# Performance work log

Hardware: AMD Instinct MI355X
Metric: run time of the kernel (lower is better)

The kernel has to match this reference:

```python
import jax, jax.numpy as jnp
import numpy as np
from jax.ops import segment_sum

N = 50000        # nodes
E = 800000       # edges (avg degree 16)
H = 128          # hidden_dim
N_ITER = 2       # BCRefinement n_iterations
TIE_P = 0.05     # fraction of tie (boundary) edges


def setup_inputs() -> dict:
    key = jax.random.key(0)
    ks = jax.random.split(key, 24)
    s = 0.02
    inp = {
        'h': jax.random.normal(ks[0], (N, H), jnp.float32),
        'e': jax.random.normal(ks[1], (E, H), jnp.float32),
        'edge_attr_raw': jax.random.normal(ks[2], (E, 10), jnp.float32),
        # edge_refine: Linear(3H,2H) -> ReLU -> Linear(2H,H)
        'W_er1': s * jax.random.normal(ks[3], (3 * H, 2 * H), jnp.float32),
        'b_er1': jnp.zeros((2 * H,), jnp.float32),
        'W_er2': s * jax.random.normal(ks[4], (2 * H, H), jnp.float32),
        'b_er2': jnp.zeros((H,), jnp.float32),
        # GRUCell(H,H) torch layout: [3H, H] chunks (r, z, n)
        'W_ih': s * jax.random.normal(ks[5], (3 * H, H), jnp.float32),
        'W_hh': s * jax.random.normal(ks[6], (3 * H, H), jnp.float32),
        'b_ih': jnp.zeros((3 * H,), jnp.float32),
        'b_hh': jnp.zeros((3 * H,), jnp.float32),
        # node_neigh_fc: Linear(H,H)
        'W_nn': s * jax.random.normal(ks[7], (H, H), jnp.float32),
        'b_nn': jnp.zeros((H,), jnp.float32),
        # gate_mlp: Linear(3H,H) -> ReLU -> Linear(H,1), last bias init -2.0
        'W_g1': s * jax.random.normal(ks[8], (3 * H, H), jnp.float32),
        'b_g1': jnp.zeros((H,), jnp.float32),
        'W_g2': s * jax.random.normal(ks[9], (H, 1), jnp.float32),
        'b_g2': jnp.full((1,), -2.0, jnp.float32),
        'edge_index': jax.random.randint(ks[10], (2, E), 0, N, jnp.int32),
        'is_tie': jax.random.uniform(ks[11], (E,)) < TIE_P,
    }
    return inp


def reference(h, e, edge_attr_raw,
              W_er1, b_er1, W_er2, b_er2,
              W_ih, W_hh, b_ih, b_hh,
              W_nn, b_nn,
              W_g1, b_g1, W_g2, b_g2,
              edge_index, is_tie):
    row = edge_index[0]
    col = edge_index[1]
    tie_f = is_tie.astype(h.dtype)                        # [E]
    internal = ~is_tie

    # coupling buses: endpoints of any tie edge (tie-incidence count > 0)
    cpl_cnt = segment_sum(tie_f, row, num_segments=N) + \
              segment_sum(tie_f, col, num_segments=N)     # [N]
    is_cpl = cpl_cnt > 0

    # internal edges pointing into coupling buses; b_smooth weights w = 1/sqrt(X^2+eps)
    to_cpl = internal & is_cpl[col]
    X = jnp.abs(edge_attr_raw[:, 1])
    w = jnp.where(to_cpl, 1.0 / jnp.sqrt(X * X + 1e-6), 0.0)
    w_den = segment_sum(w, col, num_segments=N)           # [N]
    w_norm = w / (w_den[col] + 1e-6)                      # [E], zero off-mask

    deg = jnp.maximum(cpl_cnt, 1.0)                       # clamp_min(1.0)

    h_work, e_work = h, e
    for _ in range(N_ITER):
        # --- tie-edge refinement (applied only on tie edges) ---
        edge_in = jnp.concatenate([e_work, h_work[row], h_work[col]], axis=-1)  # [E,3H]
        e_ref = jax.nn.relu(edge_in @ W_er1 + b_er1) @ W_er2 + b_er2            # [E,H]
        e_work = e_work + tie_f[:, None] * e_ref

        # --- node messages from internal neighbors into coupling buses ---
        m_node_msg = h_work[row] @ W_nn + b_nn                                   # [E,H]
        m_node_all = segment_sum(m_node_msg * w_norm[:, None], col,
                                 num_segments=N)                                 # [N,H]

        # --- mean of incident tie-edge features at each node ---
        tie_e = tie_f[:, None] * e_work                                          # [E,H]
        m_edge_all = (segment_sum(tie_e, row, num_segments=N) +
                      segment_sum(tie_e, col, num_segments=N)) / deg[:, None]    # [N,H]

        # --- gating + GRU update on coupling buses ---
        gate_in = jnp.concatenate([m_edge_all, m_node_all, h_work], axis=-1)     # [N,3H]
        gate = jax.nn.sigmoid(jax.nn.relu(gate_in @ W_g1 + b_g1) @ W_g2 + b_g2)  # [N,1]
        m = m_edge_all + gate * m_node_all                                       # [N,H]

        gi = m @ W_ih.T + b_ih                                                   # [N,3H]
        gh = h_work @ W_hh.T + b_hh
        r = jax.nn.sigmoid(gi[:, :H] + gh[:, :H])
        z = jax.nn.sigmoid(gi[:, H:2 * H] + gh[:, H:2 * H])
        n = jnp.tanh(gi[:, 2 * H:] + r * gh[:, 2 * H:])
        h_new = (1.0 - z) * n + z * h_work

        h_work = jnp.where(is_cpl[:, None], h_new, h_work)
    return h_work, e_work
```

## Files before the change

kernel.cpp:

```cpp
#include <hip/hip_runtime.h>
#include <cstdint>

#define N_NODES 50000
#define N_EDGES 800000
#define HDIM    128
#define TIE_CAP 44000
#define NITER   2
#define SCAN_B  256
#define EB_CONST 3125
#define TB_CONST 172

typedef __attribute__((ext_vector_type(8))) short bf16x8;
typedef __attribute__((ext_vector_type(4))) float f32x4;

__device__ __forceinline__ uint32_t f2bf(float f) {
    uint32_t u = __builtin_bit_cast(uint32_t, f);
    return (u + 0x7fffu + ((u >> 16) & 1u)) >> 16;
}
__device__ __forceinline__ float bf2f(uint32_t b) {
    return __builtin_bit_cast(float, b << 16);
}
__device__ __forceinline__ uint32_t comb2(uint32_t me, uint32_t mn, float g) {
    float a0 = bf2f(me & 0xffffu) + g * bf2f(mn & 0xffffu);
    float a1 = bf2f(me >> 16)     + g * bf2f(mn >> 16);
    return f2bf(a0) | (f2bf(a1) << 16);
}


__device__ __forceinline__ void stage_a128(const float* __restrict__ base,
                                           const int* __restrict__ gidx,
                                           int m0, int Mlim, char* tile, int tid)
{
    const int c = tid & 15;
    #pragma unroll
    for (int p = 0; p < 4; ++p) {
        int row = p * 32 + (tid >> 4);
        int ar = m0 + row; if (ar >= Mlim) ar = Mlim - 1;
        long g = gidx ? gidx[ar] : ar;
        const float* s = base + g * HDIM + c * 4;
        float4 v0 = *(const float4*)s;
        float4 v1 = *(const float4*)(s + 64);
        uint2 w0 = make_uint2(f2bf(v0.x) | (f2bf(v0.y) << 16),
                              f2bf(v0.z) | (f2bf(v0.w) << 16));
        uint2 w1 = make_uint2(f2bf(v1.x) | (f2bf(v1.y) << 16),
                              f2bf(v1.z) | (f2bf(v1.w) << 16));
        int sw = (row & 7) << 4;
        *(uint2*)(tile + row * 256 + ((c * 8) ^ sw)) = w0;
        *(uint2*)(tile + row * 256 + ((c * 8 + 128) ^ sw)) = w1;
    }
}

__device__ __forceinline__ void stage_bf128(const uint16_t* __restrict__ base,
                                            const int* __restrict__ gidx,
                                            int m0, int Mlim, char* tile, int tid)
{
    const int c = tid & 15;
    #pragma unroll
    for (int p = 0; p < 4; ++p) {
        int row = p * 32 + (tid >> 4);
        int ar = m0 + row; if (ar >= Mlim) ar = Mlim - 1;
        long g = gidx ? gidx[ar] : ar;
        uint4 v = *(const uint4*)(base + g * HDIM + c * 8);
        *(uint4*)(tile + row * 256 + ((c * 16) ^ ((row & 7) << 4))) = v;
    }
}

__device__ __forceinline__ void stage_b128(const short* __restrict__ BT, int ldk,
                                           int n0, int k0, char* tile, int tid)
{
    const int c = tid & 15;
    #pragma unroll
    for (int p = 0; p < 4; ++p) {
        int n = p * 32 + (tid >> 4);
        uint4 v = *(const uint4*)&BT[(size_t)(n0 + n) * ldk + k0 + c * 8];
        *(uint4*)(tile + n * 256 + ((c * 16) ^ ((n & 7) << 4))) = v;
    }
}

__device__ __forceinline__ void mfma128(const char* At, const char* Bt,
                                        int wr, int wc, int lane, f32x4 acc[4][2])
{
    #pragma unroll
    for (int ks = 0; ks < 4; ++ks) {
        int kb = ks * 64 + (lane >> 4) * 16;
        bf16x8 aF[4], bF[2];
        #pragma unroll
        for (int mi = 0; mi < 4; ++mi) {
            int row = wr * 64 + mi * 16 + (lane & 15);
            aF[mi] = *(const bf16x8*)(At + row * 256 + (kb ^ ((row & 7) << 4)));
        }
        #pragma unroll
        for (int ni = 0; ni < 2; ++ni) {
            int n = wc * 32 + ni * 16 + (lane & 15);
            bF[ni] = *(const bf16x8*)(Bt + n * 256 + (kb ^ ((n & 7) << 4)));
        }
        #pragma unroll
        for (int mi = 0; mi < 4; ++mi)
            #pragma unroll
            for (int ni = 0; ni < 2; ++ni)
                acc[mi][ni] = __builtin_amdgcn_mfma_f32_16x16x32_bf16(
                    aF[mi], bF[ni], acc[mi][ni], 0, 0, 0);
    }
}

__global__ __launch_bounds__(512)
void k_tie_fused(float* __restrict__ out_e, const uint16_t* __restrict__ h_bf,
                 const int* __restrict__ tie_cnt_p,
                 const int* __restrict__ tie_list, const int* __restrict__ tie_row,
                 const int* __restrict__ tie_col,
                 const short* __restrict__ BTer1, const short* __restrict__ BTer2,
                 const float* __restrict__ b_er1, const float* __restrict__ b_er2)
{
    int cnt = *tie_cnt_p; if (cnt > TIE_CAP) cnt = TIE_CAP;
    const int m0 = blockIdx.x * 128;
    if (m0 >= cnt) return;

    __shared__ __align__(16) char At[32 * 1024];
    __shared__ __align__(16) char B0[32 * 1024];
    __shared__ __align__(16) char B1[32 * 1024];

    const int tid = threadIdx.x, lane = tid & 63;
    const int wid = tid >> 6, wr = wid >> 2, wc = wid & 3;

    f32x4 acc0[4][2] = {}, acc1[4][2] = {};
    #pragma unroll 1
    for (int c = 0; c < 3; ++c) {
        if (c == 0) stage_a128(out_e, tie_list, m0, cnt, At, tid);
        else        stage_bf128(h_bf, (c == 1) ? tie_row : tie_col, m0, cnt, At, tid);
        stage_b128(BTer1, 384, 0,   c * 128, B0, tid);
        stage_b128(BTer1, 384, 128, c * 128, B1, tid);
        __syncthreads();
        mfma128(At, B0, wr, wc, lane, acc0);
        mfma128(At, B1, wr, wc, lane, acc1);
        __syncthreads();
    }

    #pragma unroll
    for (int half = 0; half < 2; ++half) {
        char* Ct = half ? B0 : At;
        #pragma unroll
        for (int ni = 0; ni < 2; ++ni) {
            int col = wc * 32 + ni * 16 + (lane & 15);
            float bv = b_er1[half * 128 + col];
            #pragma unroll
            for (int mi = 0; mi < 4; ++mi)
                #pragma unroll
                for (int j = 0; j < 4; ++j) {
                    int rl = wr * 64 + mi * 16 + ((lane >> 4) << 2) + j;
                    float v = fmaxf((half ? acc1 : acc0)[mi][ni][j] + bv, 0.f);
                    *(uint16_t*)(Ct + rl * 256 + ((col * 2) ^ ((rl & 7) << 4))) =
                        (uint16_t)f2bf(v);
                }
        }
    }
    stage_b128(BTer2, 256, 0, 0, B1, tid);
    __syncthreads();
    f32x4 acc2[4][2] = {};
    mfma128(At, B1, wr, wc, lane, acc2);
    __syncthreads();
    stage_b128(BTer2, 256, 0, 128, B1, tid);
    __syncthreads();
    mfma128(B0, B1, wr, wc, lane, acc2);

    int col0 = wc * 32 + (lane & 15);
    float bv0 = b_er2[col0], bv1 = b_er2[col0 + 16];
    #pragma unroll
    for (int mi = 0; mi < 4; ++mi) {
        #pragma unroll
        for (int j = 0; j < 4; ++j) {
            int i = m0 + wr * 64 + mi * 16 + ((lane >> 4) << 2) + j;
            if (i < cnt) {
                int e = tie_list[i];
                #pragma unroll
                for (int ni = 0; ni < 2; ++ni) {
                    int col = col0 + ni * 16;
                    size_t eb = (size_t)e * HDIM + col;
                    out_e[eb] += acc2[mi][ni][j] + (ni ? bv1 : bv0);
                }
            }
        }
    }
}

__global__ __launch_bounds__(256)
void k_gather(const int* __restrict__ row_ptr, const int* __restrict__ csr_row,
              const float* __restrict__ csr_w, const uint16_t* __restrict__ h_bf,
              uint16_t* __restrict__ agg,
              const int* __restrict__ row_ptr2, const int* __restrict__ tcsr,
              const float* __restrict__ out_e, const float* __restrict__ deg_inv,
              uint16_t* __restrict__ m_edge_bf)
{
    int n = blockIdx.x * 4 + (threadIdx.x >> 6);
    if (n >= N_NODES) return;
    int lane = threadIdx.x & 63;

    int s = row_ptr[n], t = row_ptr[n + 1];
    float a0 = 0.f, a1 = 0.f;
    for (int j = s; j < t; ++j) {
        int r = csr_row[j];
        float w = csr_w[j];
        uint32_t v = *(const uint32_t*)(h_bf + (size_t)r * HDIM + lane * 2);
        a0 += w * bf2f(v & 0xffffu);
        a1 += w * bf2f(v >> 16);
    }
    *(uint32_t*)(agg + (size_t)n * HDIM + lane * 2) = f2bf(a0) | (f2bf(a1) << 16);

    int s2 = row_ptr2[n], t2 = row_ptr2[n + 1];
    float b0 = 0.f, b1 = 0.f;
    for (int j = s2; j < t2; ++j) {
        int e = tcsr[j];
        float2 v = *(const float2*)(out_e + (size_t)e * HDIM + lane * 2);
        b0 += v.x; b1 += v.y;
    }
    float di = deg_inv[n];
    *(uint32_t*)(m_edge_bf + (size_t)n * HDIM + lane * 2) =
        f2bf(b0 * di) | (f2bf(b1 * di) << 16);
}

__global__ __launch_bounds__(512)
void k_node_mega(const uint16_t* __restrict__ m_edge_bf,
                 const uint16_t* __restrict__ agg,
                 float* __restrict__ out_h, uint16_t* __restrict__ h_bf,
                 const float* __restrict__ cpl_cnt, const float* __restrict__ sumw,
                 const short* __restrict__ BTnn, const float* __restrict__ b_nn,
                 const short* __restrict__ BTg1, const float* __restrict__ b_g1,
                 const float* __restrict__ Wg2, const float* __restrict__ b_g2,
                 const short* __restrict__ BTcomb,
                 const short* __restrict__ BTihn, const short* __restrict__ BThhn,
                 const float* __restrict__ b_ih, const float* __restrict__ b_hh)
{
    const int m0 = blockIdx.x * 128;
    __shared__ __align__(16) char Tme[32 * 1024];
    __shared__ __align__(16) char Tmn[32 * 1024];
    __shared__ __align__(16) char Th [32 * 1024];
    __shared__ __align__(16) char Bt [32 * 1024];
    __shared__ float g_red[4][128];
    __shared__ float g_fin[128];
    __shared__ float sw_s[128];

    const int tid = threadIdx.x, lane = tid & 63;
    const int wid = tid >> 6, wr = wid >> 2, wc = wid & 3;

    stage_bf128(m_edge_bf, nullptr, m0, N_NODES, Tme, tid);
    stage_bf128(agg,       nullptr, m0, N_NODES, Tmn, tid);
    stage_bf128(h_bf,      nullptr, m0, N_NODES, Th,  tid);
    stage_b128(BTnn, 128, 0, 0, Bt, tid);
    if (tid < 128) {
        int n = m0 + tid; if (n >= N_NODES) n = N_NODES - 1;
        sw_s[tid] = sumw[n];
    }
    __syncthreads();

    {
        f32x4 accM[4][2] = {};
        mfma128(Tmn, Bt, wr, wc, lane, accM);
        __syncthreads();
        #pragma unroll
        for (int ni = 0; ni < 2; ++ni) {
            int col = wc * 32 + ni * 16 + (lane & 15);
            float bv = b_nn[col];
            #pragma unroll
            for (int mi = 0; mi < 4; ++mi)
                #pragma unroll
                for (int j = 0; j < 4; ++j) {
                    int rl = wr * 64 + mi * 16 + ((lane >> 4) << 2) + j;
                    float v = accM[mi][ni][j] + sw_s[rl] * bv;
                    *(uint16_t*)(Tmn + rl * 256 + ((col * 2) ^ ((rl & 7) << 4))) =
                        (uint16_t)f2bf(v);
                }
        }
        __syncthreads();
    }

    f32x4 accG[4][2] = {};
    #pragma unroll 1
    for (int c = 0; c < 3; ++c) {
        const char* Ac = (c == 0) ? Tme : (c == 1) ? Tmn : Th;
        stage_b128(BTg1, 384, 0, c * 128, Bt, tid);
        __syncthreads();
        mfma128(Ac, Bt, wr, wc, lane, accG);
        __syncthreads();
    }
    {
        float bg[2], wg[2];
        #pragma unroll
        for (int ni = 0; ni < 2; ++ni) {
            int col = wc * 32 + ni * 16 + (lane & 15);
            bg[ni] = b_g1[col]; wg[ni] = Wg2[col];
        }
        #pragma unroll
        for (int mi = 0; mi < 4; ++mi)
            #pragma unroll
            for (int j = 0; j < 4; ++j) {
                float p = fmaxf(accG[mi][0][j] + bg[0], 0.f) * wg[0]
                        + fmaxf(accG[mi][1][j] + bg[1], 0.f) * wg[1];
                #pragma unroll
                for (int o = 8; o; o >>= 1) p += __shfl_xor(p, o);
                if ((lane & 15) == 0)
                    g_red[wc][wr * 64 + mi * 16 + ((lane >> 4) << 2) + j] = p;
            }
    }
    __syncthreads();
    if (tid < 128) {
        float t = g_red[0][tid] + g_red[1][tid] + g_red[2][tid] + g_red[3][tid]
                + b_g2[0];
        g_fin[tid] = 1.f / (1.f + __expf(-t));
    }
    __syncthreads();

    stage_b128(BTcomb, 256, 0, 0, Bt, tid);
    {
        const int c = tid & 15;
        #pragma unroll
        for (int p = 0; p < 4; ++p) {
            int row = p * 32 + (tid >> 4);
            float g = g_fin[row];
            int sw = (row & 7) << 4;
            #pragma unroll
            for (int hh = 0; hh < 2; ++hh) {
                int off = (c * 8 + hh * 128) ^ sw;
                uint2 me2 = *(uint2*)(Tme + row * 256 + off);
                uint2 mn2 = *(uint2*)(Tmn + row * 256 + off);
                *(uint2*)(Tmn + row * 256 + off) =
                    make_uint2(comb2(me2.x, mn2.x, g), comb2(me2.y, mn2.y, g));
            }
        }
    }
    __syncthreads();

    f32x4 aR[4][2] = {}, aZ[4][2] = {}, aGI[4][2] = {}, aGH[4][2] = {};
    stage_b128(BTcomb, 256, 0, 128, Tme, tid);
    mfma128(Tmn, Bt, wr, wc, lane, aR);   __syncthreads();
    stage_b128(BTcomb, 256, 128, 0, Bt, tid);
    mfma128(Th, Tme, wr, wc, lane, aR);   __syncthreads();
    stage_b128(BTcomb, 256, 128, 128, Tme, tid);
    mfma128(Tmn, Bt, wr, wc, lane, aZ);   __syncthreads();
    stage_b128(BTihn, 128, 0, 0, Bt, tid);
    mfma128(Th, Tme, wr, wc, lane, aZ);   __syncthreads();
    stage_b128(BThhn, 128, 0, 0, Tme, tid);
    mfma128(Tmn, Bt, wr, wc, lane, aGI);  __syncthreads();
    mfma128(Th, Tme, wr, wc, lane, aGH);

    #pragma unroll
    for (int ni = 0; ni < 2; ++ni) {
        int col = wc * 32 + ni * 16 + (lane & 15);
        float br  = b_ih[col] + b_hh[col];
        float bz  = b_ih[128 + col] + b_hh[128 + col];
        float bin = b_ih[256 + col], bhn = b_hh[256 + col];
        #pragma unroll
        for (int mi = 0; mi < 4; ++mi)
            #pragma unroll
            for (int j = 0; j < 4; ++j) {
                int node = m0 + wr * 64 + mi * 16 + ((lane >> 4) << 2) + j;
                if (node < N_NODES && cpl_cnt[node] > 0.f) {
                    float r = 1.f / (1.f + __expf(-(aR[mi][ni][j] + br)));
                    float z = 1.f / (1.f + __expf(-(aZ[mi][ni][j] + bz)));
                    float nn = tanhf(aGI[mi][ni][j] + bin + r * (aGH[mi][ni][j] + bhn));
                    size_t hb = (size_t)node * HDIM + col;
                    float hv = out_h[hb];
                    float hn = (1.f - z) * nn + z * hv;
                    out_h[hb] = hn;
                    h_bf[hb] = (uint16_t)f2bf(hn);
                }
            }
    }
}

#define INIT_BLOCKS 2497

__global__ __launch_bounds__(256)
void k_init(const float* __restrict__ e, float* __restrict__ out_e,
            const float* __restrict__ h, float* __restrict__ out_h,
            uint16_t* __restrict__ h_bf,
            float* __restrict__ cpl_cnt, float* __restrict__ w_den,
            int* __restrict__ hist, int* __restrict__ counters,
            const uint8_t* __restrict__ tie_raw,
            const float* __restrict__ W_er1, const float* __restrict__ W_er2,
            const float* __restrict__ W_nn, const float* __restrict__ W_g1,
            const float* __restrict__ W_ih, const float* __restrict__ W_hh,
            short* __restrict__ BTer1, short* __restrict__ BTer2,
            short* __restrict__ BTnn, short* __restrict__ BTg1,
            short* __restrict__ BTcomb, short* __restrict__ BTihn,
            short* __restrict__ BThhn)
{
    const int b = blockIdx.x, t = threadIdx.x;
    if (b < 2048) {
        const float4* src = (const float4*)e;
        float4* dst = (float4*)out_e;
        for (int i = b * 256 + t; i < N_EDGES * HDIM / 4; i += 2048 * 256)
            dst[i] = src[i];
    } else if (b < 2304) {
        for (int i = (b - 2048) * 256 + t; i < N_NODES * HDIM / 4; i += 256 * 256) {
            float4 v = ((const float4*)h)[i];
            ((float4*)out_h)[i] = v;
            *(uint2*)(h_bf + (size_t)i * 4) =
                make_uint2(f2bf(v.x) | (f2bf(v.y) << 16),
                           f2bf(v.z) | (f2bf(v.w) << 16));
        }
    } else if (b < 2368) {
        for (int i = (b - 2304) * 256 + t; i < N_NODES; i += 64 * 256) {
            cpl_cnt[i] = 0.f; w_den[i] = 0.f; hist[i] = 0;
        }
    } else if (b < 2496) {
        for (int i = (b - 2368) * 256 + t; i < 384 * 256; i += 128 * 256) {
            {   int n = i / 384, k = i % 384;
                BTer1[i] = (short)f2bf(W_er1[(size_t)k * 256 + n]); }
            if (i < 128 * 256) {
                int n = i / 256, k = i % 256;
                BTer2[i] = (short)f2bf(W_er2[(size_t)k * 128 + n]); }
            if (i < 128 * 128) {
                int n = i / 128, k = i % 128;
                BTnn[i] = (short)f2bf(W_nn[(size_t)k * 128 + n]); }
            if (i < 128 * 384) {
                int n = i / 384, k = i % 384;
                BTg1[i] = (short)f2bf(W_g1[(size_t)k * 128 + n]); }
            if (i < 256 * 256) {
                int n = i >> 8, k = i & 255;
                float v = (k < 128) ? W_ih[n * 128 + k] : W_hh[n * 128 + (k - 128)];
                BTcomb[i] = (short)f2bf(v); }
            if (i < 128 * 128) {
                BTihn[i] = (short)f2bf(W_ih[256 * 128 + i]);
                BThhn[i] = (short)f2bf(W_hh[256 * 128 + i]); }
        }
    } else {
        if (t < 64) {
            int c = 0;
            for (int k = t; k < 4096; k += 64)
                if ((k & 3) && tie_raw[k]) c = 1;
            unsigned long long m = __ballot(c != 0);
            if (t == 0) {
                counters[0] = (m != 0ull) ? 1 : 0;
                counters[1] = 0; counters[2] = 0; counters[3] = 0;
            }
        }
    }
}

__global__ __launch_bounds__(256)
void k_tie(const void* __restrict__ tie_raw, const int* __restrict__ counters,
           const int* __restrict__ ei, float* __restrict__ cpl_cnt,
           int* __restrict__ tie_cnt, int* __restrict__ tie_list,
           int* __restrict__ tie_row, int* __restrict__ tie_col)
{
    int e = blockIdx.x * 256 + threadIdx.x;
    int fmt = counters[0];
    bool t = false; int r = 0, c = 0;
    if (e < N_EDGES)
        t = fmt ? (((const uint8_t*)tie_raw)[e] != 0)
                : (((const int*)tie_raw)[e] != 0);
    if (t) {
        r = ei[e]; c = ei[N_EDGES + e];
        atomicAdd(&cpl_cnt[r], 1.f);
        atomicAdd(&cpl_cnt[c], 1.f);
    }
    unsigned long long m = __ballot(t);
    if (m == 0ull) return;
    int lane = threadIdx.x & 63;
    int first = __ffsll((unsigned long long)m) - 1;
    int base = 0;
    if (lane == first) base = atomicAdd(tie_cnt, __popcll(m));
    base = __shfl(base, first);
    if (t) {
        int idx = base + __popcll(m & ((1ull << lane) - 1ull));
        if (idx < TIE_CAP) { tie_list[idx] = e; tie_row[idx] = r; tie_col[idx] = c; }
    }
}

__global__ __launch_bounds__(256)
void k_w(const void* __restrict__ tie_raw, const int* __restrict__ counters,
         const int* __restrict__ ei, const float* __restrict__ attr,
         const float* __restrict__ cpl_cnt, float* __restrict__ w_den,
         float* __restrict__ w_arr, int* __restrict__ hist)
{
    int e = blockIdx.x * 256 + threadIdx.x;
    if (e >= N_EDGES) return;
    int fmt = counters[0];
    bool t = fmt ? (((const uint8_t*)tie_raw)[e] != 0)
                 : (((const int*)tie_raw)[e] != 0);
    float w = 0.f;
    if (!t) {
        int c = ei[N_EDGES + e];
        if (cpl_cnt[c] > 0.f) {
            float X = fabsf(attr[(size_t)e * 10 + 1]);
            w = 1.f / sqrtf(X * X + 1e-6f);
            atomicAdd(&w_den[c], w);
            atomicAdd(&hist[c], 1);
        }
    }
    w_arr[e] = w;
}

__global__ __launch_bounds__(SCAN_B)
void k_scan1(const int* __restrict__ hist, const float* __restrict__ cpl_cnt,
             int* __restrict__ excl, int* __restrict__ bsum,
             int* __restrict__ excl2, int* __restrict__ bsum2)
{
    __shared__ int s[SCAN_B];
    int t = threadIdx.x;
    int i = blockIdx.x * SCAN_B + t;
    int v = (i < N_NODES) ? hist[i] : 0;
    s[t] = v;
    __syncthreads();
    for (int o = 1; o < SCAN_B; o <<= 1) {
        int u = (t >= o) ? s[t - o] : 0;
        __syncthreads();
        s[t] += u;
        __syncthreads();
    }
    if (i < N_NODES) excl[i] = s[t] - v;
    if (t == SCAN_B - 1) bsum[blockIdx.x] = s[t];
    __syncthreads();
    int v2 = (i < N_NODES) ? (int)cpl_cnt[i] : 0;
    s[t] = v2;
    __syncthreads();
    for (int o = 1; o < SCAN_B; o <<= 1) {
        int u = (t >= o) ? s[t - o] : 0;
        __syncthreads();
        s[t] += u;
        __syncthreads();
    }
    if (i < N_NODES) excl2[i] = s[t] - v2;
    if (t == SCAN_B - 1) bsum2[blockIdx.x] = s[t];
}

__global__ void k_scan2(int* __restrict__ bsum, int* __restrict__ bsum2,
                        int* __restrict__ counters)
{
    const int NB = (N_NODES + SCAN_B - 1) / SCAN_B;
    if (threadIdx.x == 0) {
        int run = 0;
        for (int b = 0; b < NB; ++b) { int x = bsum[b]; bsum[b] = run; run += x; }
        counters[2] = run;
        int run2 = 0;
        for (int b = 0; b < NB; ++b) { int x = bsum2[b]; bsum2[b] = run2; run2 += x; }
        counters[3] = run2;
    }
}

__global__ __launch_bounds__(256)
void k_scan3(const int* __restrict__ excl, const int* __restrict__ bsum,
             const int* __restrict__ excl2, const int* __restrict__ bsum2,
             int* __restrict__ row_ptr, int* __restrict__ cursor,
             int* __restrict__ row_ptr2, int* __restrict__ cursor2,
             const int* __restrict__ counters,
             const float* __restrict__ cpl_cnt, const float* __restrict__ w_den,
             float* __restrict__ deg_inv, float* __restrict__ sumw)
{
    int i = blockIdx.x * 256 + threadIdx.x;
    if (i < N_NODES) {
        int v = excl[i] + bsum[i >> 8];
        row_ptr[i] = v;  cursor[i] = v;
        int v2 = excl2[i] + bsum2[i >> 8];
        row_ptr2[i] = v2; cursor2[i] = v2;
        deg_inv[i] = 1.f / fmaxf(cpl_cnt[i], 1.f);
        float wd = w_den[i];
        sumw[i] = wd / (wd + 1e-6f);
    }
    if (i == N_NODES) {
        row_ptr[N_NODES] = counters[2];
        row_ptr2[N_NODES] = counters[3];
    }
}

__global__ __launch_bounds__(256)
void k_fill(const int* __restrict__ ei, const float* __restrict__ w_arr,
            const float* __restrict__ w_den, int* __restrict__ cursor,
            int* __restrict__ csr_row, float* __restrict__ csr_w,
            const int* __restrict__ counters, const int* __restrict__ tie_list,
            const int* __restrict__ tie_row, const int* __restrict__ tie_col,
            int* __restrict__ cursor2, int* __restrict__ tcsr)
{
    int b = blockIdx.x;
    if (b < EB_CONST) {
        int e = b * 256 + threadIdx.x;
        if (e >= N_EDGES) return;
        float w = w_arr[e];
        if (w == 0.f) return;
        int c = ei[N_EDGES + e];
        int pos = atomicAdd(&cursor[c], 1);
        csr_row[pos] = ei[e];
        csr_w[pos] = w / (w_den[c] + 1e-6f);
    } else {
        int i = (b - EB_CONST) * 256 + threadIdx.x;
        int cnt = counters[1]; if (cnt > TIE_CAP) cnt = TIE_CAP;
        if (i < cnt) {
            int e = tie_list[i];
            int p1 = atomicAdd(&cursor2[tie_row[i]], 1); tcsr[p1] = e;
            int p2 = atomicAdd(&cursor2[tie_col[i]], 1); tcsr[p2] = e;
        }
    }
}

extern "C" void kernel_launch(void* const* d_in, const int* in_sizes, int n_in,
                              void* d_out, int out_size, void* d_ws, size_t ws_size,
                              hipStream_t stream)
{
    const float* h     = (const float*)d_in[0];
    const float* e     = (const float*)d_in[1];
    const float* attr  = (const float*)d_in[2];
    const float* W_er1 = (const float*)d_in[3];
    const float* b_er1 = (const float*)d_in[4];
    const float* W_er2 = (const float*)d_in[5];
    const float* b_er2 = (const float*)d_in[6];
    const float* W_ih  = (const float*)d_in[7];
    const float* W_hh  = (const float*)d_in[8];
    const float* b_ih  = (const float*)d_in[9];
    const float* b_hh  = (const float*)d_in[10];
    const float* W_nn  = (const float*)d_in[11];
    const float* b_nn  = (const float*)d_in[12];
    const float* W_g1  = (const float*)d_in[13];
    const float* b_g1  = (const float*)d_in[14];
    const float* W_g2  = (const float*)d_in[15];
    const float* b_g2  = (const float*)d_in[16];
    const int*   ei    = (const int*)d_in[17];
    const void*  tie_raw = d_in[18];

    float* out_h = (float*)d_out;
    float* out_e = out_h + (size_t)N_NODES * HDIM;

    char* ws = (char*)d_ws;
    size_t off = 0;
    auto alloc = [&](size_t bytes) -> void* {
        void* p = ws + off;
        off = (off + bytes + 255) & ~(size_t)255;
        return p;
    };
    float* cpl_cnt = (float*)alloc((size_t)N_NODES * 4);
    float* w_den   = (float*)alloc((size_t)N_NODES * 4);
    int*   hist    = (int*)  alloc((size_t)N_NODES * 4);
    int*   counters= (int*)  alloc(256);
    float* deg_inv = (float*)alloc((size_t)N_NODES * 4);
    float* sumw    = (float*)alloc((size_t)N_NODES * 4);
    float* w_arr   = (float*)alloc((size_t)N_EDGES * 4);
    int* tie_list  = (int*)alloc((size_t)TIE_CAP * 4);
    int* tie_row   = (int*)alloc((size_t)TIE_CAP * 4);
    int* tie_col   = (int*)alloc((size_t)TIE_CAP * 4);
    short* BTer1   = (short*)alloc((size_t)256 * 384 * 2);
    short* BTer2   = (short*)alloc((size_t)128 * 256 * 2);
    short* BTnn    = (short*)alloc((size_t)128 * 128 * 2);
    short* BTg1    = (short*)alloc((size_t)128 * 384 * 2);
    short* BTcomb  = (short*)alloc((size_t)256 * 256 * 2);
    short* BTihn   = (short*)alloc((size_t)128 * 128 * 2);
    short* BThhn   = (short*)alloc((size_t)128 * 128 * 2);
    uint16_t* h_bf = (uint16_t*)alloc((size_t)N_NODES * HDIM * 2);
    uint16_t* agg  = (uint16_t*)alloc((size_t)N_NODES * HDIM * 2);
    uint16_t* m_edge_bf = (uint16_t*)alloc((size_t)N_NODES * HDIM * 2);
    int* excl      = (int*)alloc((size_t)N_NODES * 4);
    int* excl2     = (int*)alloc((size_t)N_NODES * 4);
    int* bsum      = (int*)alloc(256 * 4);
    int* bsum2     = (int*)alloc(256 * 4);
    int* row_ptr   = (int*)alloc((size_t)(N_NODES + 1) * 4);
    int* row_ptr2  = (int*)alloc((size_t)(N_NODES + 1) * 4);
    int* cursor    = (int*)alloc((size_t)N_NODES * 4);
    int* cursor2   = (int*)alloc((size_t)N_NODES * 4);
    int* csr_row   = (int*)alloc((size_t)N_EDGES * 4);
    float* csr_w   = (float*)alloc((size_t)N_EDGES * 4);
    int* tcsr      = (int*)alloc((size_t)2 * TIE_CAP * 4);
    if (off > ws_size) return;

    int* tie_cnt = counters + 1;

    const int GM_T = (TIE_CAP + 127) / 128;
    const int GM_N = (N_NODES + 127) / 128;
    const int NB   = (N_NODES + SCAN_B - 1) / SCAN_B;

    k_init<<<INIT_BLOCKS, 256, 0, stream>>>(
        e, out_e, h, out_h, h_bf, cpl_cnt, w_den, hist, counters,
        (const uint8_t*)tie_raw,
        W_er1, W_er2, W_nn, W_g1, W_ih, W_hh,
        BTer1, BTer2, BTnn, BTg1, BTcomb, BTihn, BThhn);
    k_tie<<<EB_CONST, 256, 0, stream>>>(tie_raw, counters, ei, cpl_cnt,
                                        tie_cnt, tie_list, tie_row, tie_col);
    k_w<<<EB_CONST, 256, 0, stream>>>(tie_raw, counters, ei, attr, cpl_cnt,
                                      w_den, w_arr, hist);
    k_scan1<<<NB, SCAN_B, 0, stream>>>(hist, cpl_cnt, excl, bsum, excl2, bsum2);
    k_scan2<<<1, 64, 0, stream>>>(bsum, bsum2, counters);
    k_scan3<<<(N_NODES + 256) / 256, 256, 0, stream>>>(
        excl, bsum, excl2, bsum2, row_ptr, cursor, row_ptr2, cursor2,
        counters, cpl_cnt, w_den, deg_inv, sumw);
    k_fill<<<EB_CONST + TB_CONST, 256, 0, stream>>>(
        ei, w_arr, w_den, cursor, csr_row, csr_w,
        counters, tie_list, tie_row, tie_col, cursor2, tcsr);

    for (int it = 0; it < NITER; ++it) {
        k_tie_fused<<<GM_T, 512, 0, stream>>>(
            out_e, h_bf, tie_cnt, tie_list, tie_row, tie_col,
            BTer1, BTer2, b_er1, b_er2);
        k_gather<<<(N_NODES + 3) / 4, 256, 0, stream>>>(
            row_ptr, csr_row, csr_w, h_bf, agg,
            row_ptr2, tcsr, out_e, deg_inv, m_edge_bf);
        k_node_mega<<<GM_N, 512, 0, stream>>>(
            m_edge_bf, agg, out_h, h_bf, cpl_cnt, sumw,
            BTnn, b_nn, BTg1, b_g1, W_g2, b_g2,
            BTcomb, BTihn, BThhn, b_ih, b_hh);
    }
}
```

Baseline: 843.8 us.

## Copy only non-tie edges inside first tie-fused launch, read tie edges from input

Removes the full E×H copy of e into out_e from the init kernel. In the first iteration, extra blocks of the tie-edge GEMM kernel copy only internal (non-tie) edge rows, while tie edges are read directly from the original input and written as e + delta. This saves reading and writing the roughly 5% of rows that are tie edges and overlaps the copy with the tie MLP. The cost is a per-row tie flag check inside the copy loop and a copy that now runs in parallel with the GEMM work.

```diff
diff --git a/kernel.cpp b/kernel.cpp
--- a/kernel.cpp
+++ b/kernel.cpp
@@ -9,6 +9,8 @@
 #define SCAN_B  256
 #define EB_CONST 3125
 #define TB_CONST 172
+#define GM_T     344
+#define COPY_B   1664
 
 typedef __attribute__((ext_vector_type(8))) short bf16x8;
 typedef __attribute__((ext_vector_type(4))) float f32x4;
@@ -104,14 +106,32 @@
 }
 
 __global__ __launch_bounds__(512)
-void k_tie_fused(float* __restrict__ out_e, const uint16_t* __restrict__ h_bf,
-                 const int* __restrict__ tie_cnt_p,
+void k_tie_fused(const float* __restrict__ e_src, float* __restrict__ out_e,
+                 const float* __restrict__ e_orig,
+                 const void* __restrict__ tie_raw, const int* __restrict__ counters,
+                 const uint16_t* __restrict__ h_bf,
                  const int* __restrict__ tie_list, const int* __restrict__ tie_row,
                  const int* __restrict__ tie_col,
                  const short* __restrict__ BTer1, const short* __restrict__ BTer2,
                  const float* __restrict__ b_er1, const float* __restrict__ b_er2)
 {
-    int cnt = *tie_cnt_p; if (cnt > TIE_CAP) cnt = TIE_CAP;
+    const int tid = threadIdx.x;
+
+    if ((int)blockIdx.x >= GM_T) {
+        int fmt = counters[0];
+        const float4* src = (const float4*)e_orig;
+        float4* dst = (float4*)out_e;
+        for (int i = ((int)blockIdx.x - GM_T) * 512 + tid;
+             i < N_EDGES * (HDIM / 4); i += COPY_B * 512) {
+            int row = i >> 5;
+            bool t = fmt ? (((const uint8_t*)tie_raw)[row] != 0)
+                         : (((const int*)tie_raw)[row] != 0);
+            if (!t) dst[i] = src[i];
+        }
+        return;
+    }
+
+    int cnt = counters[1]; if (cnt > TIE_CAP) cnt = TIE_CAP;
     const int m0 = blockIdx.x * 128;
     if (m0 >= cnt) return;
 
@@ -119,13 +139,13 @@
     __shared__ __align__(16) char B0[32 * 1024];
     __shared__ __align__(16) char B1[32 * 1024];
 
-    const int tid = threadIdx.x, lane = tid & 63;
+    const int lane = tid & 63;
     const int wid = tid >> 6, wr = wid >> 2, wc = wid & 3;
 
     f32x4 acc0[4][2] = {}, acc1[4][2] = {};
     #pragma unroll 1
     for (int c = 0; c < 3; ++c) {
-        if (c == 0) stage_a128(out_e, tie_list, m0, cnt, At, tid);
+        if (c == 0) stage_a128(e_src, tie_list, m0, cnt, At, tid);
         else        stage_bf128(h_bf, (c == 1) ? tie_row : tie_col, m0, cnt, At, tid);
         stage_b128(BTer1, 384, 0,   c * 128, B0, tid);
         stage_b128(BTer1, 384, 128, c * 128, B1, tid);
@@ -175,7 +195,7 @@
                 for (int ni = 0; ni < 2; ++ni) {
                     int col = col0 + ni * 16;
                     size_t eb = (size_t)e * HDIM + col;
-                    out_e[eb] += acc2[mi][ni][j] + (ni ? bv1 : bv0);
+                    out_e[eb] = e_src[eb] + acc2[mi][ni][j] + (ni ? bv1 : bv0);
                 }
             }
         }
@@ -366,11 +386,10 @@
     }
 }
 
-#define INIT_BLOCKS 2497
+#define INIT_BLOCKS 449
 
 __global__ __launch_bounds__(256)
-void k_init(const float* __restrict__ e, float* __restrict__ out_e,
-            const float* __restrict__ h, float* __restrict__ out_h,
+void k_init(const float* __restrict__ h, float* __restrict__ out_h,
             uint16_t* __restrict__ h_bf,
             float* __restrict__ cpl_cnt, float* __restrict__ w_den,
             int* __restrict__ hist, int* __restrict__ counters,
@@ -384,25 +403,20 @@
             short* __restrict__ BThhn)
 {
     const int b = blockIdx.x, t = threadIdx.x;
-    if (b < 2048) {
-        const float4* src = (const float4*)e;
-        float4* dst = (float4*)out_e;
-        for (int i = b * 256 + t; i < N_EDGES * HDIM / 4; i += 2048 * 256)
-            dst[i] = src[i];
-    } else if (b < 2304) {
-        for (int i = (b - 2048) * 256 + t; i < N_NODES * HDIM / 4; i += 256 * 256) {
+    if (b < 256) {
+        for (int i = b * 256 + t; i < N_NODES * HDIM / 4; i += 256 * 256) {
             float4 v = ((const float4*)h)[i];
             ((float4*)out_h)[i] = v;
             *(uint2*)(h_bf + (size_t)i * 4) =
                 make_uint2(f2bf(v.x) | (f2bf(v.y) << 16),
                            f2bf(v.z) | (f2bf(v.w) << 16));
         }
-    } else if (b < 2368) {
-        for (int i = (b - 2304) * 256 + t; i < N_NODES; i += 64 * 256) {
+    } else if (b < 320) {
+        for (int i = (b - 256) * 256 + t; i < N_NODES; i += 64 * 256) {
             cpl_cnt[i] = 0.f; w_den[i] = 0.f; hist[i] = 0;
         }
-    } else if (b < 2496) {
-        for (int i = (b - 2368) * 256 + t; i < 384 * 256; i += 128 * 256) {
+    } else if (b < 448) {
+        for (int i = (b - 320) * 256 + t; i < 384 * 256; i += 128 * 256) {
             {   int n = i / 384, k = i % 384;
                 BTer1[i] = (short)f2bf(W_er1[(size_t)k * 256 + n]); }
             if (i < 128 * 256) {
@@ -658,19 +672,16 @@
     int* tcsr      = (int*)alloc((size_t)2 * TIE_CAP * 4);
     if (off > ws_size) return;
 
-    int* tie_cnt = counters + 1;
-
-    const int GM_T = (TIE_CAP + 127) / 128;
     const int GM_N = (N_NODES + 127) / 128;
     const int NB   = (N_NODES + SCAN_B - 1) / SCAN_B;
 
     k_init<<<INIT_BLOCKS, 256, 0, stream>>>(
-        e, out_e, h, out_h, h_bf, cpl_cnt, w_den, hist, counters,
+        h, out_h, h_bf, cpl_cnt, w_den, hist, counters,
         (const uint8_t*)tie_raw,
         W_er1, W_er2, W_nn, W_g1, W_ih, W_hh,
         BTer1, BTer2, BTnn, BTg1, BTcomb, BTihn, BThhn);
     k_tie<<<EB_CONST, 256, 0, stream>>>(tie_raw, counters, ei, cpl_cnt,
-                                        tie_cnt, tie_list, tie_row, tie_col);
+                                        counters + 1, tie_list, tie_row, tie_col);
     k_w<<<EB_CONST, 256, 0, stream>>>(tie_raw, counters, ei, attr, cpl_cnt,
                                       w_den, w_arr, hist);
     k_scan1<<<NB, SCAN_B, 0, stream>>>(hist, cpl_cnt, excl, bsum, excl2, bsum2);
@@ -683,8 +694,11 @@
         counters, tie_list, tie_row, tie_col, cursor2, tcsr);
 
     for (int it = 0; it < NITER; ++it) {
-        k_tie_fused<<<GM_T, 512, 0, stream>>>(
-            out_e, h_bf, tie_cnt, tie_list, tie_row, tie_col,
+        const float* e_src = (it == 0) ? e : out_e;
+        int grid = (it == 0) ? (GM_T + COPY_B) : GM_T;
+        k_tie_fused<<<grid, 512, 0, stream>>>(
+            e_src, out_e, e, tie_raw, counters, h_bf,
+            tie_list, tie_row, tie_col,
             BTer1, BTer2, b_er1, b_er2);
         k_gather<<<(N_NODES + 3) / 4, 256, 0, stream>>>(
             row_ptr, csr_row, csr_w, h_bf, agg,
```

New measurement: 979.7 us. 16.1% more time.

## Double-buffer A tiles in tie-edge MLP kernel and read e directly on first iteration

Applied to the files above, without the earlier changes.

The tie-edge MLP kernel now uses two A-tile shared buffers, so the gather of the next 128-wide input chunk overlaps with the MFMA work on the current chunk. The loop over the three chunks is unrolled, and the second-layer weight chunks are staged while the ReLU hidden tile is being written. The kernel also takes a separate source pointer, which on the first iteration is the original e. This sets up skipping the copy of e into out_e, but init still appears to do that copy. Shared memory rises from 96KB to 128KB per block, which may reduce occupancy.

```diff
diff --git a/kernel.cpp b/kernel.cpp
--- a/kernel.cpp
+++ b/kernel.cpp
@@ -104,18 +104,20 @@
 }
 
 __global__ __launch_bounds__(512)
-void k_tie_fused(float* __restrict__ out_e, const uint16_t* __restrict__ h_bf,
-                 const int* __restrict__ tie_cnt_p,
+void k_tie_fused(const float* __restrict__ e_src, float* __restrict__ out_e,
+                 const int* __restrict__ counters,
+                 const uint16_t* __restrict__ h_bf,
                  const int* __restrict__ tie_list, const int* __restrict__ tie_row,
                  const int* __restrict__ tie_col,
                  const short* __restrict__ BTer1, const short* __restrict__ BTer2,
                  const float* __restrict__ b_er1, const float* __restrict__ b_er2)
 {
-    int cnt = *tie_cnt_p; if (cnt > TIE_CAP) cnt = TIE_CAP;
+    int cnt = counters[1]; if (cnt > TIE_CAP) cnt = TIE_CAP;
     const int m0 = blockIdx.x * 128;
     if (m0 >= cnt) return;
 
-    __shared__ __align__(16) char At[32 * 1024];
+    __shared__ __align__(16) char At0[32 * 1024];
+    __shared__ __align__(16) char At1[32 * 1024];
     __shared__ __align__(16) char B0[32 * 1024];
     __shared__ __align__(16) char B1[32 * 1024];
 
@@ -123,21 +125,37 @@
     const int wid = tid >> 6, wr = wid >> 2, wc = wid & 3;
 
     f32x4 acc0[4][2] = {}, acc1[4][2] = {};
-    #pragma unroll 1
-    for (int c = 0; c < 3; ++c) {
-        if (c == 0) stage_a128(out_e, tie_list, m0, cnt, At, tid);
-        else        stage_bf128(h_bf, (c == 1) ? tie_row : tie_col, m0, cnt, At, tid);
-        stage_b128(BTer1, 384, 0,   c * 128, B0, tid);
-        stage_b128(BTer1, 384, 128, c * 128, B1, tid);
-        __syncthreads();
-        mfma128(At, B0, wr, wc, lane, acc0);
-        mfma128(At, B1, wr, wc, lane, acc1);
-        __syncthreads();
-    }
-
+
+    stage_a128(e_src, tie_list, m0, cnt, At0, tid);
+    stage_b128(BTer1, 384, 0,   0, B0, tid);
+    stage_b128(BTer1, 384, 128, 0, B1, tid);
+    __syncthreads();
+
+    stage_bf128(h_bf, tie_row, m0, cnt, At1, tid);
+    mfma128(At0, B0, wr, wc, lane, acc0);
+    mfma128(At0, B1, wr, wc, lane, acc1);
+    __syncthreads();
+    stage_b128(BTer1, 384, 0,   128, B0, tid);
+    stage_b128(BTer1, 384, 128, 128, B1, tid);
+    __syncthreads();
+
+    stage_bf128(h_bf, tie_col, m0, cnt, At0, tid);
+    mfma128(At1, B0, wr, wc, lane, acc0);
+    mfma128(At1, B1, wr, wc, lane, acc1);
+    __syncthreads();
+    stage_b128(BTer1, 384, 0,   256, B0, tid);
+    stage_b128(BTer1, 384, 128, 256, B1, tid);
+    __syncthreads();
+
+    mfma128(At0, B0, wr, wc, lane, acc0);
+    mfma128(At0, B1, wr, wc, lane, acc1);
+    __syncthreads();
+
+    stage_b128(BTer2, 256, 0, 0,   B0, tid);
+    stage_b128(BTer2, 256, 0, 128, B1, tid);
     #pragma unroll
     for (int half = 0; half < 2; ++half) {
-        char* Ct = half ? B0 : At;
+        char* Ct = half ? At0 : At1;
         #pragma unroll
         for (int ni = 0; ni < 2; ++ni) {
             int col = wc * 32 + ni * 16 + (lane & 15);
@@ -153,14 +171,11 @@
                 }
         }
     }
-    stage_b128(BTer2, 256, 0, 0, B1, tid);
-    __syncthreads();
+    __syncthreads();
+
     f32x4 acc2[4][2] = {};
-    mfma128(At, B1, wr, wc, lane, acc2);
-    __syncthreads();
-    stage_b128(BTer2, 256, 0, 128, B1, tid);
-    __syncthreads();
-    mfma128(B0, B1, wr, wc, lane, acc2);
+    mfma128(At1, B0, wr, wc, lane, acc2);
+    mfma128(At0, B1, wr, wc, lane, acc2);
 
     int col0 = wc * 32 + (lane & 15);
     float bv0 = b_er2[col0], bv1 = b_er2[col0 + 16];
@@ -175,7 +190,7 @@
                 for (int ni = 0; ni < 2; ++ni) {
                     int col = col0 + ni * 16;
                     size_t eb = (size_t)e * HDIM + col;
-                    out_e[eb] += acc2[mi][ni][j] + (ni ? bv1 : bv0);
+                    out_e[eb] = e_src[eb] + acc2[mi][ni][j] + (ni ? bv1 : bv0);
                 }
             }
         }
@@ -658,8 +673,6 @@
     int* tcsr      = (int*)alloc((size_t)2 * TIE_CAP * 4);
     if (off > ws_size) return;
 
-    int* tie_cnt = counters + 1;
-
     const int GM_T = (TIE_CAP + 127) / 128;
     const int GM_N = (N_NODES + 127) / 128;
     const int NB   = (N_NODES + SCAN_B - 1) / SCAN_B;
@@ -670,7 +683,7 @@
         W_er1, W_er2, W_nn, W_g1, W_ih, W_hh,
         BTer1, BTer2, BTnn, BTg1, BTcomb, BTihn, BThhn);
     k_tie<<<EB_CONST, 256, 0, stream>>>(tie_raw, counters, ei, cpl_cnt,
-                                        tie_cnt, tie_list, tie_row, tie_col);
+                                        counters + 1, tie_list, tie_row, tie_col);
     k_w<<<EB_CONST, 256, 0, stream>>>(tie_raw, counters, ei, attr, cpl_cnt,
                                       w_den, w_arr, hist);
     k_scan1<<<NB, SCAN_B, 0, stream>>>(hist, cpl_cnt, excl, bsum, excl2, bsum2);
@@ -683,8 +696,9 @@
         counters, tie_list, tie_row, tie_col, cursor2, tcsr);
 
     for (int it = 0; it < NITER; ++it) {
+        const float* e_src = (it == 0) ? e : out_e;
         k_tie_fused<<<GM_T, 512, 0, stream>>>(
-            out_e, h_bf, tie_cnt, tie_list, tie_row, tie_col,
+            e_src, out_e, counters, h_bf, tie_list, tie_row, tie_col,
             BTer1, BTer2, b_er1, b_er2);
         k_gather<<<(N_NODES + 3) / 4, 256, 0, stream>>>(
             row_ptr, csr_row, csr_w, h_bf, agg,
```

Measured after the change: 853.4 us. No clear change (+1.1%).

## Compact coupling-bus node list and restrict gather and node update to it

Applied to the files above, without the earlier changes.

k_scan3 now builds a compacted list of coupling nodes (nodes with any incident tie edge) using a wave ballot and one atomic per wave. k_gather and k_node_mega index through this list, so they skip nodes whose hidden state the reference leaves unchanged. The indirection costs extra index loads and gives less contiguous tile staging. The tie-edge kernel also now takes a separate source pointer, so the first iteration reads the original e instead of doing a read-modify-write on out_e.

```diff
diff --git a/kernel.cpp b/kernel.cpp
--- a/kernel.cpp
+++ b/kernel.cpp
@@ -104,14 +104,15 @@
 }
 
 __global__ __launch_bounds__(512)
-void k_tie_fused(float* __restrict__ out_e, const uint16_t* __restrict__ h_bf,
-                 const int* __restrict__ tie_cnt_p,
+void k_tie_fused(const float* __restrict__ e_src, float* __restrict__ out_e,
+                 const int* __restrict__ counters,
+                 const uint16_t* __restrict__ h_bf,
                  const int* __restrict__ tie_list, const int* __restrict__ tie_row,
                  const int* __restrict__ tie_col,
                  const short* __restrict__ BTer1, const short* __restrict__ BTer2,
                  const float* __restrict__ b_er1, const float* __restrict__ b_er2)
 {
-    int cnt = *tie_cnt_p; if (cnt > TIE_CAP) cnt = TIE_CAP;
+    int cnt = counters[1]; if (cnt > TIE_CAP) cnt = TIE_CAP;
     const int m0 = blockIdx.x * 128;
     if (m0 >= cnt) return;
 
@@ -125,7 +126,7 @@
     f32x4 acc0[4][2] = {}, acc1[4][2] = {};
     #pragma unroll 1
     for (int c = 0; c < 3; ++c) {
-        if (c == 0) stage_a128(out_e, tie_list, m0, cnt, At, tid);
+        if (c == 0) stage_a128(e_src, tie_list, m0, cnt, At, tid);
         else        stage_bf128(h_bf, (c == 1) ? tie_row : tie_col, m0, cnt, At, tid);
         stage_b128(BTer1, 384, 0,   c * 128, B0, tid);
         stage_b128(BTer1, 384, 128, c * 128, B1, tid);
@@ -175,7 +176,7 @@
                 for (int ni = 0; ni < 2; ++ni) {
                     int col = col0 + ni * 16;
                     size_t eb = (size_t)e * HDIM + col;
-                    out_e[eb] += acc2[mi][ni][j] + (ni ? bv1 : bv0);
+                    out_e[eb] = e_src[eb] + acc2[mi][ni][j] + (ni ? bv1 : bv0);
                 }
             }
         }
@@ -183,15 +184,17 @@
 }
 
 __global__ __launch_bounds__(256)
-void k_gather(const int* __restrict__ row_ptr, const int* __restrict__ csr_row,
+void k_gather(const int* __restrict__ cpl_list, const int* __restrict__ counters,
+              const int* __restrict__ row_ptr, const int* __restrict__ csr_row,
               const float* __restrict__ csr_w, const uint16_t* __restrict__ h_bf,
               uint16_t* __restrict__ agg,
               const int* __restrict__ row_ptr2, const int* __restrict__ tcsr,
               const float* __restrict__ out_e, const float* __restrict__ deg_inv,
               uint16_t* __restrict__ m_edge_bf)
 {
-    int n = blockIdx.x * 4 + (threadIdx.x >> 6);
-    if (n >= N_NODES) return;
+    int idx = blockIdx.x * 4 + (threadIdx.x >> 6);
+    if (idx >= counters[4]) return;
+    int n = cpl_list[idx];
     int lane = threadIdx.x & 63;
 
     int s = row_ptr[n], t = row_ptr[n + 1];
@@ -218,10 +221,11 @@
 }
 
 __global__ __launch_bounds__(512)
-void k_node_mega(const uint16_t* __restrict__ m_edge_bf,
+void k_node_mega(const int* __restrict__ cpl_list, const int* __restrict__ counters,
+                 const uint16_t* __restrict__ m_edge_bf,
                  const uint16_t* __restrict__ agg,
                  float* __restrict__ out_h, uint16_t* __restrict__ h_bf,
-                 const float* __restrict__ cpl_cnt, const float* __restrict__ sumw,
+                 const float* __restrict__ sumw,
                  const short* __restrict__ BTnn, const float* __restrict__ b_nn,
                  const short* __restrict__ BTg1, const float* __restrict__ b_g1,
                  const float* __restrict__ Wg2, const float* __restrict__ b_g2,
@@ -229,7 +233,10 @@
                  const short* __restrict__ BTihn, const short* __restrict__ BThhn,
                  const float* __restrict__ b_ih, const float* __restrict__ b_hh)
 {
+    const int ncpl = counters[4];
     const int m0 = blockIdx.x * 128;
+    if (m0 >= ncpl) return;
+
     __shared__ __align__(16) char Tme[32 * 1024];
     __shared__ __align__(16) char Tmn[32 * 1024];
     __shared__ __align__(16) char Th [32 * 1024];
@@ -241,13 +248,13 @@
     const int tid = threadIdx.x, lane = tid & 63;
     const int wid = tid >> 6, wr = wid >> 2, wc = wid & 3;
 
-    stage_bf128(m_edge_bf, nullptr, m0, N_NODES, Tme, tid);
-    stage_bf128(agg,       nullptr, m0, N_NODES, Tmn, tid);
-    stage_bf128(h_bf,      nullptr, m0, N_NODES, Th,  tid);
+    stage_bf128(m_edge_bf, cpl_list, m0, ncpl, Tme, tid);
+    stage_bf128(agg,       cpl_list, m0, ncpl, Tmn, tid);
+    stage_bf128(h_bf,      cpl_list, m0, ncpl, Th,  tid);
     stage_b128(BTnn, 128, 0, 0, Bt, tid);
     if (tid < 128) {
-        int n = m0 + tid; if (n >= N_NODES) n = N_NODES - 1;
-        sw_s[tid] = sumw[n];
+        int i = m0 + tid; if (i >= ncpl) i = ncpl - 1;
+        sw_s[tid] = sumw[cpl_list[i]];
     }
     __syncthreads();
 
@@ -351,8 +358,9 @@
         for (int mi = 0; mi < 4; ++mi)
             #pragma unroll
             for (int j = 0; j < 4; ++j) {
-                int node = m0 + wr * 64 + mi * 16 + ((lane >> 4) << 2) + j;
-                if (node < N_NODES && cpl_cnt[node] > 0.f) {
+                int i = m0 + wr * 64 + mi * 16 + ((lane >> 4) << 2) + j;
+                if (i < ncpl) {
+                    int node = cpl_list[i];
                     float r = 1.f / (1.f + __expf(-(aR[mi][ni][j] + br)));
                     float z = 1.f / (1.f + __expf(-(aZ[mi][ni][j] + bz)));
                     float nn = tanhf(aGI[mi][ni][j] + bin + r * (aGH[mi][ni][j] + bhn));
@@ -431,6 +439,7 @@
             if (t == 0) {
                 counters[0] = (m != 0ull) ? 1 : 0;
                 counters[1] = 0; counters[2] = 0; counters[3] = 0;
+                counters[4] = 0;
             }
         }
     }
@@ -542,12 +551,15 @@
              const int* __restrict__ excl2, const int* __restrict__ bsum2,
              int* __restrict__ row_ptr, int* __restrict__ cursor,
              int* __restrict__ row_ptr2, int* __restrict__ cursor2,
-             const int* __restrict__ counters,
+             int* __restrict__ counters,
              const float* __restrict__ cpl_cnt, const float* __restrict__ w_den,
-             float* __restrict__ deg_inv, float* __restrict__ sumw)
+             float* __restrict__ deg_inv, float* __restrict__ sumw,
+             int* __restrict__ cpl_list)
 {
     int i = blockIdx.x * 256 + threadIdx.x;
-    if (i < N_NODES) {
+    bool in = (i < N_NODES);
+    bool cpl = false;
+    if (in) {
         int v = excl[i] + bsum[i >> 8];
         row_ptr[i] = v;  cursor[i] = v;
         int v2 = excl2[i] + bsum2[i >> 8];
@@ -555,10 +567,21 @@
         deg_inv[i] = 1.f / fmaxf(cpl_cnt[i], 1.f);
         float wd = w_den[i];
         sumw[i] = wd / (wd + 1e-6f);
+        cpl = (cpl_cnt[i] > 0.f);
     }
     if (i == N_NODES) {
         row_ptr[N_NODES] = counters[2];
         row_ptr2[N_NODES] = counters[3];
+    }
+    unsigned long long m = __ballot(cpl);
+    if (m) {
+        int lane = threadIdx.x & 63;
+        int first = __ffsll((unsigned long long)m) - 1;
+        int base = 0;
+        if (lane == first) base = atomicAdd(&counters[4], __popcll(m));
+        base = __shfl(base, first);
+        if (cpl)
+            cpl_list[base + __popcll(m & ((1ull << lane) - 1ull))] = i;
     }
 }
 
@@ -656,9 +679,8 @@
     int* csr_row   = (int*)alloc((size_t)N_EDGES * 4);
     float* csr_w   = (float*)alloc((size_t)N_EDGES * 4);
     int* tcsr      = (int*)alloc((size_t)2 * TIE_CAP * 4);
+    int* cpl_list  = (int*)alloc((size_t)N_NODES * 4);
     if (off > ws_size) return;
-
-    int* tie_cnt = counters + 1;
 
     const int GM_T = (TIE_CAP + 127) / 128;
     const int GM_N = (N_NODES + 127) / 128;
@@ -670,27 +692,28 @@
         W_er1, W_er2, W_nn, W_g1, W_ih, W_hh,
         BTer1, BTer2, BTnn, BTg1, BTcomb, BTihn, BThhn);
     k_tie<<<EB_CONST, 256, 0, stream>>>(tie_raw, counters, ei, cpl_cnt,
-                                        tie_cnt, tie_list, tie_row, tie_col);
+                                        counters + 1, tie_list, tie_row, tie_col);
     k_w<<<EB_CONST, 256, 0, stream>>>(tie_raw, counters, ei, attr, cpl_cnt,
                                       w_den, w_arr, hist);
     k_scan1<<<NB, SCAN_B, 0, stream>>>(hist, cpl_cnt, excl, bsum, excl2, bsum2);
     k_scan2<<<1, 64, 0, stream>>>(bsum, bsum2, counters);
     k_scan3<<<(N_NODES + 256) / 256, 256, 0, stream>>>(
         excl, bsum, excl2, bsum2, row_ptr, cursor, row_ptr2, cursor2,
-        counters, cpl_cnt, w_den, deg_inv, sumw);
+        counters, cpl_cnt, w_den, deg_inv, sumw, cpl_list);
     k_fill<<<EB_CONST + TB_CONST, 256, 0, stream>>>(
         ei, w_arr, w_den, cursor, csr_row, csr_w,
         counters, tie_list, tie_row, tie_col, cursor2, tcsr);
 
     for (int it = 0; it < NITER; ++it) {
+        const float* e_src = (it == 0) ? e : out_e;
         k_tie_fused<<<GM_T, 512, 0, stream>>>(
-            out_e, h_bf, tie_cnt, tie_list, tie_row, tie_col,
+            e_src, out_e, counters, h_bf, tie_list, tie_row, tie_col,
             BTer1, BTer2, b_er1, b_er2);
         k_gather<<<(N_NODES + 3) / 4, 256, 0, stream>>>(
-            row_ptr, csr_row, csr_w, h_bf, agg,
+            cpl_list, counters, row_ptr, csr_row, csr_w, h_bf, agg,
             row_ptr2, tcsr, out_e, deg_inv, m_edge_bf);
         k_node_mega<<<GM_N, 512, 0, stream>>>(
-            m_edge_bf, agg, out_h, h_bf, cpl_cnt, sumw,
+            cpl_list, counters, m_edge_bf, agg, out_h, h_bf, sumw,
             BTnn, b_nn, BTg1, b_g1, W_g2, b_g2,
             BTcomb, BTihn, BThhn, b_ih, b_hh);
     }
```

After: 847.0 us. Within noise of the previous version (+0.4%).
